# Kernel optimization log

Hardware: AMD Instinct MI355X
Metric: run time of the kernel (lower is better)

The kernel has to match this reference:

```python
import jax, jax.numpy as jnp
import numpy as np

B, T, C = 4, 2048, 2048
D_ATT, D_FFN = 2048, 8192
EPS = 1e-5

def setup_inputs() -> dict:
    key = jax.random.key(0)
    ks = jax.random.split(key, 20)
    n = lambda k, s, sc=0.02: jax.random.normal(k, s, dtype=jnp.float32) * sc
    u = lambda k, s: jax.random.uniform(k, s, dtype=jnp.float32)
    return {
        'x': jax.random.normal(ks[0], (B, T, C), dtype=jnp.float32),
        'ln1_w': jnp.ones((C,), jnp.float32), 'ln1_b': jnp.zeros((C,), jnp.float32),
        'ln2_w': jnp.ones((C,), jnp.float32), 'ln2_b': jnp.zeros((C,), jnp.float32),
        'tm_k': u(ks[1], (1, 1, C)), 'tm_v': u(ks[2], (1, 1, C)), 'tm_r': u(ks[3], (1, 1, C)),
        'time_decay': n(ks[4], (D_ATT,), 1.0),            # raw; decay = -exp(time_decay)
        'time_first': n(ks[5], (D_ATT,), 0.3) + float(np.log(0.3)),
        'Wk': n(ks[6], (D_ATT, C)), 'Wv': n(ks[7], (D_ATT, C)),
        'Wr': n(ks[8], (D_ATT, C)), 'Wo': n(ks[9], (C, D_ATT)),
        'cm_k': u(ks[10], (1, 1, C)), 'cm_r': u(ks[11], (1, 1, C)),
        'Wck': n(ks[12], (D_FFN, C)), 'Wcv': n(ks[13], (C, D_FFN)), 'Wcr': n(ks[14], (C, C)),
    }

def layer_norm(x, w, b):
    mu = jnp.mean(x, axis=-1, keepdims=True)
    var = jnp.var(x, axis=-1, keepdims=True)
    return (x - mu) * jax.lax.rsqrt(var + EPS) * w + b

def time_shift(x):
    # xx[:, t] = x[:, t-1], zero at t=0
    return jnp.pad(x, ((0, 0), (1, 0), (0, 0)))[:, :-1]

def wkv(time_decay, time_first, k, v):
    # Numerically-stable WKV linear recurrence (RWKV-4). k, v: [B,T,D]
    decay = -jnp.exp(time_decay)  # [D]
    kT = jnp.swapaxes(k, 0, 1)    # [T,B,D]
    vT = jnp.swapaxes(v, 0, 1)

    def step(carry, kv_t):
        aa, bb, pp = carry
        kt, vt = kv_t
        ww = time_first + kt
        p = jnp.maximum(pp, ww)
        e1 = jnp.exp(pp - p)
        e2 = jnp.exp(ww - p)
        out = (e1 * aa + e2 * vt) / (e1 * bb + e2)
        ww2 = pp + decay
        p2 = jnp.maximum(ww2, kt)
        e1b = jnp.exp(ww2 - p2)
        e2b = jnp.exp(kt - p2)
        return (e1b * aa + e2b * vt, e1b * bb + e2b, p2), out

    z = jnp.zeros((k.shape[0], k.shape[2]), k.dtype)
    init = (z, z, jnp.full_like(z, -1e38))
    _, outT = jax.lax.scan(step, init, (kT, vT))
    return jnp.swapaxes(outT, 0, 1)  # [B,T,D]

def reference(x, ln1_w, ln1_b, ln2_w, ln2_b, tm_k, tm_v, tm_r,
              time_decay, time_first, Wk, Wv, Wr, Wo,
              cm_k, cm_r, Wck, Wcv, Wcr):
    # --- TimeMix ---
    h = layer_norm(x, ln1_w, ln1_b)
    hh = time_shift(h)
    xk = h * tm_k + hh * (1 - tm_k)
    xv = h * tm_v + hh * (1 - tm_v)
    xr = h * tm_r + hh * (1 - tm_r)
    k = jnp.einsum('btc,dc->btd', xk, Wk)
    v = jnp.einsum('btc,dc->btd', xv, Wv)
    sr = jax.nn.sigmoid(jnp.einsum('btc,dc->btd', xr, Wr))
    rwkv = sr * wkv(time_decay, time_first, k, v)
    x = x + jnp.einsum('btd,cd->btc', rwkv, Wo)
    # --- ChannelMix ---
    g = layer_norm(x, ln2_w, ln2_b)
    gg = time_shift(g)
    xk2 = g * cm_k + gg * (1 - cm_k)
    xr2 = g * cm_r + gg * (1 - cm_r)
    kf = jnp.square(jax.nn.relu(jnp.einsum('btc,fc->btf', xk2, Wck)))
    kv = jnp.einsum('btf,cf->btc', kf, Wcv)
    x = x + jax.nn.sigmoid(jnp.einsum('btc,dc->btd', xr2, Wcr)) * kv
    return x
```

## Files before the change

### kernel.cpp

```cpp
#include <hip/hip_runtime.h>
#include <hip/hip_bf16.h>

#define B_ 4
#define T_ 2048
#define C_ 2048
#define D_ 2048
#define F_ 8192
#define BT_ (B_*T_)
#define NCH 64
#define LCH 32

using bf16 = __hip_bfloat16;
typedef __attribute__((ext_vector_type(8))) short bf16x8;
typedef __attribute__((ext_vector_type(4))) float f32x4;

template<bool V> struct BC { static constexpr bool value = V; };

struct bf4 { bf16 a, b, c, d; };

__device__ __forceinline__ bf4 to_bf4(float x, float y, float z, float w) {
  bf4 r;
  r.a = __float2bfloat16(x); r.b = __float2bfloat16(y);
  r.c = __float2bfloat16(z); r.d = __float2bfloat16(w);
  return r;
}

__global__ __launch_bounds__(256) void cvt_kernel(const float* __restrict__ in,
                                                  bf16* __restrict__ out, int n4) {
  int i = blockIdx.x * blockDim.x + threadIdx.x;
  int stride = gridDim.x * blockDim.x;
  for (; i < n4; i += stride) {
    float4 v = ((const float4*)in)[i];
    ((bf4*)out)[i] = to_bf4(v.x, v.y, v.z, v.w);
  }
}

__global__ __launch_bounds__(256) void cvt4_kernel(
    const float* __restrict__ in0, const float* __restrict__ in1,
    const float* __restrict__ in2, const float* __restrict__ in3,
    bf16* __restrict__ o0, bf16* __restrict__ o1,
    bf16* __restrict__ o2, bf16* __restrict__ o3, int n4) {
  const int sub = blockIdx.x >> 10;
  const int lb = blockIdx.x & 1023;
  const float* in = (sub == 0) ? in0 : (sub == 1) ? in1 : (sub == 2) ? in2 : in3;
  bf16* out = (sub == 0) ? o0 : (sub == 1) ? o1 : (sub == 2) ? o2 : o3;
  int i = lb * blockDim.x + threadIdx.x;
  int stride = 1024 * blockDim.x;
  for (; i < n4; i += stride) {
    float4 v = ((const float4*)in)[i];
    ((bf4*)out)[i] = to_bf4(v.x, v.y, v.z, v.w);
  }
}

__global__ __launch_bounds__(256) void packcvt_kernel(const float* __restrict__ in,
    bf16* __restrict__ out, int rows, int cols_out, int ld_in, int col0) {
  int n4 = rows * (cols_out >> 2);
  int c4 = cols_out >> 2;
  int i = blockIdx.x * blockDim.x + threadIdx.x;
  int stride = gridDim.x * blockDim.x;
  for (; i < n4; i += stride) {
    int r = i / c4;
    int j4 = i - r * c4;
    float4 v = *(const float4*)(in + (size_t)r * ld_in + col0 + j4 * 4);
    ((bf4*)out)[i] = to_bf4(v.x, v.y, v.z, v.w);
  }
}

__device__ __forceinline__ void block_reduce4(float v[4], float out[4]) {
  #pragma unroll
  for (int i = 0; i < 4; ++i)
    #pragma unroll
    for (int off = 1; off < 64; off <<= 1)
      v[i] += __shfl_xor(v[i], off);
  __shared__ float red[4][4];
  int wave = threadIdx.x >> 6, lane = threadIdx.x & 63;
  if (lane == 0) {
    red[wave][0] = v[0]; red[wave][1] = v[1];
    red[wave][2] = v[2]; red[wave][3] = v[3];
  }
  __syncthreads();
  #pragma unroll
  for (int i = 0; i < 4; ++i)
    out[i] = red[0][i] + red[1][i] + red[2][i] + red[3][i];
}

__global__ __launch_bounds__(256) void mix1f_kernel(const float* __restrict__ x,
    const float* __restrict__ w, const float* __restrict__ b,
    const float* __restrict__ tmk, const float* __restrict__ tmv, const float* __restrict__ tmr,
    bf16* __restrict__ xk, bf16* __restrict__ xv, bf16* __restrict__ xr) {
  const int row = blockIdx.x;
  const int t = row & (T_ - 1);
  const bool hasPrev = (t != 0);
  const int tid = threadIdx.x;
  const float* xc = x + (size_t)row * C_;
  const float* xp = xc - C_;
  float c[8], p[8];
  *(float4*)&c[0] = *(const float4*)(xc + tid * 4);
  *(float4*)&c[4] = *(const float4*)(xc + tid * 4 + 1024);
  if (hasPrev) {
    *(float4*)&p[0] = *(const float4*)(xp + tid * 4);
    *(float4*)&p[4] = *(const float4*)(xp + tid * 4 + 1024);
  } else {
    #pragma unroll
    for (int j = 0; j < 8; ++j) p[j] = 0.f;
  }
  float v[4] = {0.f, 0.f, 0.f, 0.f}, tot[4];
  #pragma unroll
  for (int j = 0; j < 8; ++j) {
    v[0] += c[j]; v[1] += c[j] * c[j];
    v[2] += p[j]; v[3] += p[j] * p[j];
  }
  block_reduce4(v, tot);
  const float muc = tot[0] * (1.f / C_);
  const float rsc = rsqrtf(tot[1] * (1.f / C_) - muc * muc + 1e-5f);
  const float mup = tot[2] * (1.f / C_);
  const float rsp = rsqrtf(tot[3] * (1.f / C_) - mup * mup + 1e-5f);
  float wv[8], bv[8], mk[8], mv[8], mr[8];
  #pragma unroll
  for (int half = 0; half < 2; ++half) {
    int i = tid * 4 + half * 1024;
    *(float4*)&wv[half*4] = *(const float4*)(w + i);
    *(float4*)&bv[half*4] = *(const float4*)(b + i);
    *(float4*)&mk[half*4] = *(const float4*)(tmk + i);
    *(float4*)&mv[half*4] = *(const float4*)(tmv + i);
    *(float4*)&mr[half*4] = *(const float4*)(tmr + i);
  }
  float ok[8], ov[8], orr[8];
  #pragma unroll
  for (int j = 0; j < 8; ++j) {
    float h  = (c[j] - muc) * rsc * wv[j] + bv[j];
    float hh = hasPrev ? ((p[j] - mup) * rsp * wv[j] + bv[j]) : 0.f;
    ok[j]  = hh + mk[j] * (h - hh);
    ov[j]  = hh + mv[j] * (h - hh);
    orr[j] = hh + mr[j] * (h - hh);
  }
  size_t ro = (size_t)row * C_;
  #pragma unroll
  for (int half = 0; half < 2; ++half) {
    int i = tid * 4 + half * 1024;
    *(bf4*)(xk + ro + i) = to_bf4(ok[half*4], ok[half*4+1], ok[half*4+2], ok[half*4+3]);
    *(bf4*)(xv + ro + i) = to_bf4(ov[half*4], ov[half*4+1], ov[half*4+2], ov[half*4+3]);
    *(bf4*)(xr + ro + i) = to_bf4(orr[half*4], orr[half*4+1], orr[half*4+2], orr[half*4+3]);
  }
}

__global__ __launch_bounds__(256) void mix2f_kernel(const float* __restrict__ x,
    const float* __restrict__ w, const float* __restrict__ b,
    const float* __restrict__ cmk, const float* __restrict__ cmr,
    bf16* __restrict__ xk2, bf16* __restrict__ xr2) {
  const int row = blockIdx.x;
  const int t = row & (T_ - 1);
  const bool hasPrev = (t != 0);
  const int tid = threadIdx.x;
  const float* xc = x + (size_t)row * C_;
  const float* xp = xc - C_;
  float c[8], p[8];
  *(float4*)&c[0] = *(const float4*)(xc + tid * 4);
  *(float4*)&c[4] = *(const float4*)(xc + tid * 4 + 1024);
  if (hasPrev) {
    *(float4*)&p[0] = *(const float4*)(xp + tid * 4);
    *(float4*)&p[4] = *(const float4*)(xp + tid * 4 + 1024);
  } else {
    #pragma unroll
    for (int j = 0; j < 8; ++j) p[j] = 0.f;
  }
  float v[4] = {0.f, 0.f, 0.f, 0.f}, tot[4];
  #pragma unroll
  for (int j = 0; j < 8; ++j) {
    v[0] += c[j]; v[1] += c[j] * c[j];
    v[2] += p[j]; v[3] += p[j] * p[j];
  }
  block_reduce4(v, tot);
  const float muc = tot[0] * (1.f / C_);
  const float rsc = rsqrtf(tot[1] * (1.f / C_) - muc * muc + 1e-5f);
  const float mup = tot[2] * (1.f / C_);
  const float rsp = rsqrtf(tot[3] * (1.f / C_) - mup * mup + 1e-5f);
  float wv[8], bv[8], mk[8], mr[8];
  #pragma unroll
  for (int half = 0; half < 2; ++half) {
    int i = tid * 4 + half * 1024;
    *(float4*)&wv[half*4] = *(const float4*)(w + i);
    *(float4*)&bv[half*4] = *(const float4*)(b + i);
    *(float4*)&mk[half*4] = *(const float4*)(cmk + i);
    *(float4*)&mr[half*4] = *(const float4*)(cmr + i);
  }
  float ok[8], orr[8];
  #pragma unroll
  for (int j = 0; j < 8; ++j) {
    float h  = (c[j] - muc) * rsc * wv[j] + bv[j];
    float hh = hasPrev ? ((p[j] - mup) * rsp * wv[j] + bv[j]) : 0.f;
    ok[j]  = hh + mk[j] * (h - hh);
    orr[j] = hh + mr[j] * (h - hh);
  }
  size_t ro = (size_t)row * C_;
  #pragma unroll
  for (int half = 0; half < 2; ++half) {
    int i = tid * 4 + half * 1024;
    *(bf4*)(xk2 + ro + i) = to_bf4(ok[half*4], ok[half*4+1], ok[half*4+2], ok[half*4+3]);
    *(bf4*)(xr2 + ro + i) = to_bf4(orr[half*4], orr[half*4+1], orr[half*4+2], orr[half*4+3]);
  }
}

__global__ __launch_bounds__(256) void wkv_pass1(
    const bf16* __restrict__ kp, const bf16* __restrict__ vp,
    const float* __restrict__ td,
    float* __restrict__ sA, float* __restrict__ sB, float* __restrict__ sP) {
  const int g = blockIdx.x * 256 + threadIdx.x;
  const int d = g & (D_ - 1);
  const int c = (g >> 11) & (NCH - 1);
  const int b = g >> 17;
  const float w = -__expf(td[d]);
  const size_t base = ((size_t)b * T_ + c * LCH) * D_ + d;
  float aa = 0.f, bb = 0.f, pp = -1e38f;
  #pragma unroll 4
  for (int j = 0; j < LCH; ++j) {
    float kt = __bfloat162float(kp[base + (size_t)j * D_]);
    float vt = __bfloat162float(vp[base + (size_t)j * D_]);
    float ww2 = pp + w;
    float p2 = fmaxf(ww2, kt);
    float e1 = __expf(ww2 - p2), e2 = __expf(kt - p2);
    aa = e1 * aa + e2 * vt;
    bb = e1 * bb + e2;
    pp = p2;
  }
  const int sidx = ((b * NCH + c) << 11) + d;
  sA[sidx] = aa; sB[sidx] = bb; sP[sidx] = pp;
}

__global__ __launch_bounds__(256) void wkv_pass2(
    const float* __restrict__ td,
    float* __restrict__ sA, float* __restrict__ sB, float* __restrict__ sP) {
  const int g = blockIdx.x * 256 + threadIdx.x;
  const int d = g & (D_ - 1);
  const int b = g >> 11;
  const float wL = -__expf(td[d]) * (float)LCH;
  float aa = 0.f, bb = 0.f, pp = -1e38f;
  for (int c = 0; c < NCH; ++c) {
    const int sidx = ((b * NCH + c) << 11) + d;
    float la = sA[sidx], lb = sB[sidx], lp = sP[sidx];
    sA[sidx] = aa; sB[sidx] = bb; sP[sidx] = pp;
    float ww2 = pp + wL;
    float q = fmaxf(ww2, lp);
    float e1 = __expf(ww2 - q), e2 = __expf(lp - q);
    aa = e1 * aa + e2 * la;
    bb = e1 * bb + e2 * lb;
    pp = q;
  }
}

__global__ __launch_bounds__(256) void wkv_pass3(
    const bf16* __restrict__ kp, const bf16* __restrict__ vp, const bf16* __restrict__ rp,
    const float* __restrict__ td, const float* __restrict__ tfp,
    const float* __restrict__ sA, const float* __restrict__ sB, const float* __restrict__ sP,
    bf16* __restrict__ rwkv) {
  const int g = blockIdx.x * 256 + threadIdx.x;
  const int d = g & (D_ - 1);
  const int c = (g >> 11) & (NCH - 1);
  const int b = g >> 17;
  const float w = -__expf(td[d]);
  const float u = tfp[d];
  const int sidx = ((b * NCH + c) << 11) + d;
  float aa = sA[sidx], bb = sB[sidx], pp = sP[sidx];
  const size_t base = ((size_t)b * T_ + c * LCH) * D_ + d;
  #pragma unroll 4
  for (int j = 0; j < LCH; ++j) {
    float kt = __bfloat162float(kp[base + (size_t)j * D_]);
    float vt = __bfloat162float(vp[base + (size_t)j * D_]);
    float rt = __bfloat162float(rp[base + (size_t)j * D_]);
    float ww = u + kt;
    float p = fmaxf(pp, ww);
    float e1 = __expf(pp - p);
    float e2 = __expf(ww - p);
    float outv = (e1 * aa + e2 * vt) / (e1 * bb + e2);
    float sr = 1.f / (1.f + __expf(-rt));
    rwkv[base + (size_t)j * D_] = __float2bfloat16(sr * outv);
    float ww2 = pp + w;
    float p2 = fmaxf(ww2, kt);
    float e1b = __expf(ww2 - p2);
    float e2b = __expf(kt - p2);
    aa = e1b * aa + e2b * vt;
    bb = e1b * bb + e2b;
    pp = p2;
  }
}

template<int EPI>
__device__ __forceinline__ void gemm_core(
    const bf16* __restrict__ A, const bf16* __restrict__ Bt,
    int N, int K, int id, int nwg,
    float* __restrict__ outF, bf16* __restrict__ outB,
    const float* __restrict__ addP, const bf16* __restrict__ sigP,
    char* lds) {
  const int tid = threadIdx.x;
  const int wid = tid >> 6, lane = tid & 63;
  const int wm = wid >> 2, wn = wid & 3;

  const int cpx = nwg >> 3;
  const int sid = (id & 7) * cpx + (id >> 3);
  const int nx = N >> 8;
  const int band = sid / (4 * nx);
  const int rem = sid - band * (4 * nx);
  const int bx = rem >> 2;
  const int by = band * 4 + (rem & 3);
  const int tileM = by * 256, tileN = bx * 256;

  const int NT = K >> 6;

  const int srow_lo = wid * 8 + (lane >> 3);
  const int scel = ((lane & 7) ^ (lane >> 3)) << 3;

  const bf16* pA[2][2];
  const bf16* pB[2][2];
  #pragma unroll
  for (int h = 0; h < 2; ++h)
    #pragma unroll
    for (int j = 0; j < 2; ++j) {
      pA[h][j] = A  + (size_t)(tileM + h * 128 + srow_lo + j * 64) * K + scel;
      pB[h][j] = Bt + (size_t)(tileN + h * 128 + srow_lo + j * 64) * K + scel;
    }
  const int ldsW = wid * 1024;

  auto stA = [&](int par, int h) {
    #pragma unroll
    for (int j = 0; j < 2; ++j) {
      __builtin_amdgcn_global_load_lds(
          (const __attribute__((address_space(1))) void*)pA[h][j],
          (__attribute__((address_space(3))) void*)(lds + par * 32768 + h * 16384 + j * 8192 + ldsW),
          16, 0, 0);
      pA[h][j] += 64;
    }
  };
  auto stB = [&](int par, int h) {
    #pragma unroll
    for (int j = 0; j < 2; ++j) {
      __builtin_amdgcn_global_load_lds(
          (const __attribute__((address_space(1))) void*)pB[h][j],
          (__attribute__((address_space(3))) void*)(lds + 65536 + par * 32768 + h * 16384 + j * 8192 + ldsW),
          16, 0, 0);
      pB[h][j] += 64;
    }
  };

  const int lane15 = lane & 15;
  const int kswz0 = ((lane >> 4) * 16) ^ ((lane & 7) << 4);
  const int aBase = (wm * 128 + lane15) * 128;
  const int bBase = (wn * 64 + lane15) * 128;

  f32x4 acc[8][4] = {};

  stB(0, 0); stB(0, 1); stA(0, 0); stA(0, 1); stB(1, 0); stB(1, 1);
  asm volatile("s_waitcnt vmcnt(4)" : : : "memory");
  __builtin_amdgcn_s_barrier();
  __builtin_amdgcn_sched_barrier(0);

  auto tileBody = [&](int t, auto doa, auto dob) {
    constexpr bool DOA = decltype(doa)::value;
    constexpr bool DOB = decltype(dob)::value;
    const char* Ab = lds + ((t & 1) << 15);
    const char* Bb = lds + 65536 + ((t & 1) << 15);
    const int parA = (t + 1) & 1;
    const int parB = t & 1;
    bf16x8 bfr[4][2];
    #pragma unroll
    for (int q = 0; q < 4; ++q) {
      if (q == 0) {
        #pragma unroll
        for (int n = 0; n < 4; ++n) {
          bfr[n][0] = *(const bf16x8*)(Bb + bBase + n * 2048 + kswz0);
          bfr[n][1] = *(const bf16x8*)(Bb + bBase + n * 2048 + (kswz0 ^ 64));
        }
      }
      bf16x8 am[2][2];
      #pragma unroll
      for (int mm = 0; mm < 2; ++mm) {
        am[mm][0] = *(const bf16x8*)(Ab + aBase + q * 4096 + mm * 2048 + kswz0);
        am[mm][1] = *(const bf16x8*)(Ab + aBase + q * 4096 + mm * 2048 + (kswz0 ^ 64));
      }
      if constexpr (DOA) {
        if (q == 0) stA(parA, 0);
        if (q == 1) stA(parA, 1);
      }
      if constexpr (DOB) {
        if (q == 2) stB(parB, 0);
        if (q == 3) stB(parB, 1);
      }
      if (q == 0)
        asm volatile("s_waitcnt lgkmcnt(8)" : : : "memory");
      __builtin_amdgcn_sched_barrier(0);
      __builtin_amdgcn_s_barrier();
      __builtin_amdgcn_sched_barrier(0);
      __builtin_amdgcn_s_setprio(1);
      #pragma unroll
      for (int kk = 0; kk < 2; ++kk)
        #pragma unroll
        for (int n = 0; n < 4; ++n) {
          acc[2*q+0][n] = __builtin_amdgcn_mfma_f32_16x16x32_bf16(am[0][kk], bfr[n][kk], acc[2*q+0][n], 0, 0, 0);
          acc[2*q+1][n] = __builtin_amdgcn_mfma_f32_16x16x32_bf16(am[1][kk], bfr[n][kk], acc[2*q+1][n], 0, 0, 0);
        }
      __builtin_amdgcn_s_setprio(0);
      __builtin_amdgcn_sched_barrier(0);
      if (q == 3) {
        if constexpr (DOB)      asm volatile("s_waitcnt vmcnt(4)" : : : "memory");
        else if constexpr (DOA) asm volatile("s_waitcnt vmcnt(0)" : : : "memory");
      }
      __builtin_amdgcn_s_barrier();
      __builtin_amdgcn_sched_barrier(0);
    }
  };

  for (int t = 0; t < NT - 2; ++t) tileBody(t, BC<true>{}, BC<true>{});
  tileBody(NT - 2, BC<true>{}, BC<false>{});
  tileBody(NT - 1, BC<false>{}, BC<false>{});

  const int erow0 = tileM + wm * 128 + (lane >> 4) * 4;
  const int ecol0 = tileN + wn * 64 + lane15;
  #pragma unroll
  for (int m = 0; m < 8; ++m) {
    #pragma unroll
    for (int n = 0; n < 4; ++n) {
      #pragma unroll
      for (int r = 0; r < 4; ++r) {
        const int grow = erow0 + m * 16 + r;
        const int gcol = ecol0 + n * 16;
        const size_t idx = (size_t)grow * N + gcol;
        const float val = acc[m][n][r];
        if constexpr (EPI == 0) {
          outB[idx] = __float2bfloat16(val);
        } else if constexpr (EPI == 1) {
          float tt = fmaxf(val, 0.f);
          outB[idx] = __float2bfloat16(tt * tt);
        } else if constexpr (EPI == 2) {
          outF[idx] = addP[idx] + val;
        } else if constexpr (EPI == 3) {
          outB[idx] = __float2bfloat16(1.f / (1.f + __expf(-val)));
        } else {
          outF[idx] = addP[idx] + __bfloat162float(sigP[idx]) * val;
        }
      }
    }
  }
}

template<int EPI>
__global__ __launch_bounds__(512, 2) void gemm256(
    const bf16* __restrict__ A, const bf16* __restrict__ Bt,
    int N, int K,
    float* __restrict__ outF, bf16* __restrict__ outB,
    const float* __restrict__ addP, const bf16* __restrict__ sigP) {
  __shared__ alignas(16) char lds[131072];
  gemm_core<EPI>(A, Bt, N, K, blockIdx.x, gridDim.x, outF, outB, addP, sigP, lds);
}

__global__ __launch_bounds__(512, 2) void gemm_kvr(
    const bf16* __restrict__ A0, const bf16* __restrict__ A1, const bf16* __restrict__ A2,
    const bf16* __restrict__ B0, const bf16* __restrict__ B1, const bf16* __restrict__ B2,
    bf16* __restrict__ O0, bf16* __restrict__ O1, bf16* __restrict__ O2) {
  __shared__ alignas(16) char lds[131072];
  const int sub = blockIdx.x >> 8;
  const int bid = blockIdx.x & 255;
  const bf16* A  = (sub == 0) ? A0 : (sub == 1) ? A1 : A2;
  const bf16* Bt = (sub == 0) ? B0 : (sub == 1) ? B1 : B2;
  bf16* O        = (sub == 0) ? O0 : (sub == 1) ? O1 : O2;
  gemm_core<0>(A, Bt, D_, C_, bid, 256, nullptr, O, nullptr, nullptr, lds);
}

extern "C" void kernel_launch(void* const* d_in, const int* in_sizes, int n_in,
                              void* d_out, int out_size, void* d_ws, size_t ws_size,
                              hipStream_t stream) {
  const float* x    = (const float*)d_in[0];
  const float* ln1w = (const float*)d_in[1];
  const float* ln1b = (const float*)d_in[2];
  const float* ln2w = (const float*)d_in[3];
  const float* ln2b = (const float*)d_in[4];
  const float* tmk  = (const float*)d_in[5];
  const float* tmv  = (const float*)d_in[6];
  const float* tmr  = (const float*)d_in[7];
  const float* td   = (const float*)d_in[8];
  const float* tf   = (const float*)d_in[9];
  const float* Wk   = (const float*)d_in[10];
  const float* Wv   = (const float*)d_in[11];
  const float* Wr   = (const float*)d_in[12];
  const float* Wo   = (const float*)d_in[13];
  const float* cmk  = (const float*)d_in[14];
  const float* cmr  = (const float*)d_in[15];
  const float* Wck  = (const float*)d_in[16];
  const float* Wcv  = (const float*)d_in[17];
  const float* Wcr  = (const float*)d_in[18];
  float* out = (float*)d_out;

  char* ws = (char*)d_ws;
  const size_t MB = 1ull << 20;
  bf16* R0 = (bf16*)(ws + 0 * MB);
  bf16* R1 = (bf16*)(ws + 32 * MB);
  bf16* R2 = (bf16*)(ws + 64 * MB);
  bf16* R3 = (bf16*)(ws + 96 * MB);
  bf16* R4 = (bf16*)(ws + 128 * MB);

  int S = (ws_size >= 256 * MB) ? 1 : (ws_size >= 192 * MB ? 2 : 4);
  const int FS = F_ / S;

  bf16* xk = R1, *xv = R2, *xr = R3;
  bf16* k_ = R4, *v_ = R1, *r_ = R2, *rwkv = R3;
  bf16* xk2 = R1, *xr2 = R2, *sig = R3, *kf = R4;

  bf16* Wk_b = R0;
  bf16* Wv_b = R0 + (size_t)D_ * C_;
  bf16* Wr_b = R0 + (size_t)2 * D_ * C_;
  bf16* Wo_b = R0 + (size_t)3 * D_ * C_;

  float* sA = (float*)R0;
  float* sB = sA + (size_t)B_ * NCH * D_;
  float* sP = sB + (size_t)B_ * NCH * D_;

  const int gN2k = (BT_ / 256) * (D_ / 256);

  mix1f_kernel<<<BT_, 256, 0, stream>>>(x, ln1w, ln1b, tmk, tmv, tmr, xk, xv, xr);
  cvt4_kernel<<<4096, 256, 0, stream>>>(Wk, Wv, Wr, Wo, Wk_b, Wv_b, Wr_b, Wo_b, D_ * C_ / 4);
  gemm_kvr<<<768, 512, 0, stream>>>(xk, xv, xr, Wk_b, Wv_b, Wr_b, k_, v_, r_);
  wkv_pass1<<<B_ * NCH * D_ / 256, 256, 0, stream>>>(k_, v_, td, sA, sB, sP);
  wkv_pass2<<<B_ * D_ / 256, 256, 0, stream>>>(td, sA, sB, sP);
  wkv_pass3<<<B_ * NCH * D_ / 256, 256, 0, stream>>>(k_, v_, r_, td, tf, sA, sB, sP, rwkv);
  gemm256<2><<<gN2k, 512, 0, stream>>>(rwkv, Wo_b, C_, D_, out, nullptr, x, nullptr);

  mix2f_kernel<<<BT_, 256, 0, stream>>>(out, ln2w, ln2b, cmk, cmr, xk2, xr2);
  cvt_kernel<<<1024, 256, 0, stream>>>(Wcr, R0, C_ * C_ / 4);
  gemm256<3><<<gN2k, 512, 0, stream>>>(xr2, R0, C_, C_, nullptr, sig, nullptr, nullptr);
  for (int h = 0; h < S; ++h) {
    cvt_kernel<<<1024, 256, 0, stream>>>(Wck + (size_t)h * FS * C_, R0, FS * C_ / 4);
    gemm256<1><<<(BT_/256) * (FS/256), 512, 0, stream>>>(xk2, R0, FS, C_, nullptr, kf, nullptr, nullptr);
    packcvt_kernel<<<1024, 256, 0, stream>>>(Wcv, R0, C_, FS, F_, h * FS);
    gemm256<4><<<gN2k, 512, 0, stream>>>(kf, R0, C_, FS, out, nullptr, out, sig);
  }
}
```

Before: 947.7 us.

## Unsplit FFN GEMMs, merge weight conversions, and use static load offsets in GEMM

The channel-mix FFN now always runs as a single full-width GEMM pair instead of splitting along F based on workspace size. The Wcr and Wck conversions are merged into one launch, Wcv is converted directly without column packing, and the converted weights are placed in separate workspace regions. Inside the GEMM, the main loop is unrolled by two so LDS parity and global-load offsets are compile-time immediates instead of per-tile pointer increments. The change assumes enough workspace for the full-size buffers and overwrites regions that were previously reused, so aliasing has to stay correct.

```diff
diff --git a/kernel.cpp b/kernel.cpp
--- a/kernel.cpp
+++ b/kernel.cpp
@@ -52,17 +52,21 @@
   }
 }
 
-__global__ __launch_bounds__(256) void packcvt_kernel(const float* __restrict__ in,
-    bf16* __restrict__ out, int rows, int cols_out, int ld_in, int col0) {
-  int n4 = rows * (cols_out >> 2);
-  int c4 = cols_out >> 2;
-  int i = blockIdx.x * blockDim.x + threadIdx.x;
-  int stride = gridDim.x * blockDim.x;
-  for (; i < n4; i += stride) {
-    int r = i / c4;
-    int j4 = i - r * c4;
-    float4 v = *(const float4*)(in + (size_t)r * ld_in + col0 + j4 * 4);
-    ((bf4*)out)[i] = to_bf4(v.x, v.y, v.z, v.w);
+__global__ __launch_bounds__(256) void cvt2w_kernel(
+    const float* __restrict__ in0, bf16* __restrict__ o0, int n40,
+    const float* __restrict__ in1, bf16* __restrict__ o1, int n41) {
+  if (blockIdx.x < 512) {
+    int i = blockIdx.x * 256 + threadIdx.x;
+    for (; i < n40; i += 512 * 256) {
+      float4 v = ((const float4*)in0)[i];
+      ((bf4*)o0)[i] = to_bf4(v.x, v.y, v.z, v.w);
+    }
+  } else {
+    int i = (blockIdx.x - 512) * 256 + threadIdx.x;
+    for (; i < n41; i += 2048 * 256) {
+      float4 v = ((const float4*)in1)[i];
+      ((bf4*)o1)[i] = to_bf4(v.x, v.y, v.z, v.w);
+    }
   }
 }
 
@@ -320,25 +324,21 @@
     }
   const int ldsW = wid * 1024;
 
-  auto stA = [&](int par, int h) {
-    #pragma unroll
-    for (int j = 0; j < 2; ++j) {
+  auto stA = [&](int par, int h, int eo) {
+    #pragma unroll
+    for (int j = 0; j < 2; ++j)
       __builtin_amdgcn_global_load_lds(
-          (const __attribute__((address_space(1))) void*)pA[h][j],
+          (const __attribute__((address_space(1))) void*)(pA[h][j] + eo),
           (__attribute__((address_space(3))) void*)(lds + par * 32768 + h * 16384 + j * 8192 + ldsW),
           16, 0, 0);
-      pA[h][j] += 64;
-    }
   };
-  auto stB = [&](int par, int h) {
-    #pragma unroll
-    for (int j = 0; j < 2; ++j) {
+  auto stB = [&](int par, int h, int eo) {
+    #pragma unroll
+    for (int j = 0; j < 2; ++j)
       __builtin_amdgcn_global_load_lds(
-          (const __attribute__((address_space(1))) void*)pB[h][j],
+          (const __attribute__((address_space(1))) void*)(pB[h][j] + eo),
           (__attribute__((address_space(3))) void*)(lds + 65536 + par * 32768 + h * 16384 + j * 8192 + ldsW),
           16, 0, 0);
-      pB[h][j] += 64;
-    }
   };
 
   const int lane15 = lane & 15;
@@ -348,18 +348,16 @@
 
   f32x4 acc[8][4] = {};
 
-  stB(0, 0); stB(0, 1); stA(0, 0); stA(0, 1); stB(1, 0); stB(1, 1);
+  stB(0, 0, 0); stB(0, 1, 0); stA(0, 0, 0); stA(0, 1, 0); stB(1, 0, 64); stB(1, 1, 64);
   asm volatile("s_waitcnt vmcnt(4)" : : : "memory");
   __builtin_amdgcn_s_barrier();
   __builtin_amdgcn_sched_barrier(0);
 
-  auto tileBody = [&](int t, auto doa, auto dob) {
+  auto tileBody = [&](int par, auto doa, auto dob, int aEo, int bEo) {
     constexpr bool DOA = decltype(doa)::value;
     constexpr bool DOB = decltype(dob)::value;
-    const char* Ab = lds + ((t & 1) << 15);
-    const char* Bb = lds + 65536 + ((t & 1) << 15);
-    const int parA = (t + 1) & 1;
-    const int parB = t & 1;
+    const char* Ab = lds + (par << 15);
+    const char* Bb = lds + 65536 + (par << 15);
     bf16x8 bfr[4][2];
     #pragma unroll
     for (int q = 0; q < 4; ++q) {
@@ -377,12 +375,12 @@
         am[mm][1] = *(const bf16x8*)(Ab + aBase + q * 4096 + mm * 2048 + (kswz0 ^ 64));
       }
       if constexpr (DOA) {
-        if (q == 0) stA(parA, 0);
-        if (q == 1) stA(parA, 1);
+        if (q == 0) stA(par ^ 1, 0, aEo);
+        if (q == 1) stA(par ^ 1, 1, aEo);
       }
       if constexpr (DOB) {
-        if (q == 2) stB(parB, 0);
-        if (q == 3) stB(parB, 1);
+        if (q == 2) stB(par, 0, bEo);
+        if (q == 3) stB(par, 1, bEo);
       }
       if (q == 0)
         asm volatile("s_waitcnt lgkmcnt(8)" : : : "memory");
@@ -408,9 +406,16 @@
     }
   };
 
-  for (int t = 0; t < NT - 2; ++t) tileBody(t, BC<true>{}, BC<true>{});
-  tileBody(NT - 2, BC<true>{}, BC<false>{});
-  tileBody(NT - 1, BC<false>{}, BC<false>{});
+  for (int t = 0; t < NT - 2; t += 2) {
+    tileBody(0, BC<true>{}, BC<true>{}, 64, 128);
+    tileBody(1, BC<true>{}, BC<true>{}, 128, 192);
+    #pragma unroll
+    for (int h = 0; h < 2; ++h)
+      #pragma unroll
+      for (int j = 0; j < 2; ++j) { pA[h][j] += 128; pB[h][j] += 128; }
+  }
+  tileBody(0, BC<true>{}, BC<false>{}, 64, 0);
+  tileBody(1, BC<false>{}, BC<false>{}, 0, 0);
 
   const int erow0 = tileM + wm * 128 + (lane >> 4) * 4;
   const int ecol0 = tileN + wn * 64 + lane15;
@@ -496,9 +501,6 @@
   bf16* R3 = (bf16*)(ws + 96 * MB);
   bf16* R4 = (bf16*)(ws + 128 * MB);
 
-  int S = (ws_size >= 256 * MB) ? 1 : (ws_size >= 192 * MB ? 2 : 4);
-  const int FS = F_ / S;
-
   bf16* xk = R1, *xv = R2, *xr = R3;
   bf16* k_ = R4, *v_ = R1, *r_ = R2, *rwkv = R3;
   bf16* xk2 = R1, *xr2 = R2, *sig = R3, *kf = R4;
@@ -511,6 +513,10 @@
   float* sA = (float*)R0;
   float* sB = sA + (size_t)B_ * NCH * D_;
   float* sP = sB + (size_t)B_ * NCH * D_;
+
+  bf16* Wcr_b = R4;
+  bf16* Wck_b = R0;
+  bf16* Wcv_b = R2;
 
   const int gN2k = (BT_ / 256) * (D_ / 256);
 
@@ -523,12 +529,9 @@
   gemm256<2><<<gN2k, 512, 0, stream>>>(rwkv, Wo_b, C_, D_, out, nullptr, x, nullptr);
 
   mix2f_kernel<<<BT_, 256, 0, stream>>>(out, ln2w, ln2b, cmk, cmr, xk2, xr2);
-  cvt_kernel<<<1024, 256, 0, stream>>>(Wcr, R0, C_ * C_ / 4);
-  gemm256<3><<<gN2k, 512, 0, stream>>>(xr2, R0, C_, C_, nullptr, sig, nullptr, nullptr);
-  for (int h = 0; h < S; ++h) {
-    cvt_kernel<<<1024, 256, 0, stream>>>(Wck + (size_t)h * FS * C_, R0, FS * C_ / 4);
-    gemm256<1><<<(BT_/256) * (FS/256), 512, 0, stream>>>(xk2, R0, FS, C_, nullptr, kf, nullptr, nullptr);
-    packcvt_kernel<<<1024, 256, 0, stream>>>(Wcv, R0, C_, FS, F_, h * FS);
-    gemm256<4><<<gN2k, 512, 0, stream>>>(kf, R0, C_, FS, out, nullptr, out, sig);
-  }
-}
+  cvt2w_kernel<<<2560, 256, 0, stream>>>(Wcr, Wcr_b, C_ * C_ / 4, Wck, Wck_b, F_ * C_ / 4);
+  gemm256<3><<<gN2k, 512, 0, stream>>>(xr2, Wcr_b, C_, C_, nullptr, sig, nullptr, nullptr);
+  cvt_kernel<<<2048, 256, 0, stream>>>(Wcv, Wcv_b, C_ * F_ / 4);
+  gemm256<1><<<(BT_/256) * (F_/256), 512, 0, stream>>>(xk2, Wck_b, F_, C_, nullptr, kf, nullptr, nullptr);
+  gemm256<4><<<gN2k, 512, 0, stream>>>(kf, Wcv_b, C_, F_, out, nullptr, out, sig);
+}
```

New measurement: 929.0 us. 1.02x faster.
